# Performance work log

Hardware: AMD Instinct MI355X
Metric: run time of the kernel (lower is better)

The kernel has to match this reference:

```python
import jax, jax.numpy as jnp
import numpy as np

N = 100000          # nodes
E = 1_600_000       # edges (avg degree 16)
K_PLUS_1 = 2        # K = 1
IN_C = 64
OUT_C = 64


def setup_inputs() -> dict:
    key = jax.random.key(0)
    ks = jax.random.split(key, 7)
    X_real = jax.random.normal(ks[0], (N, IN_C), jnp.float32)
    X_imag = jax.random.normal(ks[1], (N, IN_C), jnp.float32)
    deg_scale = np.float32(1.0 / np.sqrt(16.0))  # keep spmm output O(1), like a normalized Laplacian
    L_real_vals = jax.random.normal(ks[2], (K_PLUS_1, E), jnp.float32) * deg_scale
    L_imag_vals = jax.random.normal(ks[3], (K_PLUS_1, E), jnp.float32) * deg_scale
    edge_row = jnp.sort(jax.random.randint(ks[4], (E,), 0, N))
    edge_col = jax.random.randint(ks[5], (E,), 0, N)
    stdv = np.float32(1.0 / np.sqrt(OUT_C))
    weight = jax.random.uniform(ks[6], (K_PLUS_1, IN_C, OUT_C), jnp.float32, -stdv, stdv)
    bias = jnp.zeros((1, OUT_C), jnp.float32)
    return {
        "X_real": X_real, "X_imag": X_imag,
        "L_real_vals": L_real_vals, "L_imag_vals": L_imag_vals,
        "weight": weight, "bias": bias,
        "edge_row": edge_row, "edge_col": edge_col,
    }


def reference(X_real, X_imag, L_real_vals, L_imag_vals, weight, bias, edge_row, edge_col):
    # spmm(L_i, X): gather source features, scale by edge value, scatter-add to rows
    def spmm(vals, X):
        return jax.ops.segment_sum(vals[:, None] * X[edge_col], edge_row, num_segments=N)

    def term(lr, li, w):
        # (Lr Xr) W + (-Li Xi) W == (Lr Xr - Li Xi) W  (same math as original, fused)
        real = jnp.matmul(spmm(lr, X_real) - spmm(li, X_imag), w)
        imag = jnp.matmul(spmm(li, X_real) + spmm(lr, X_imag), w)
        return real, imag

    real_k, imag_k = jax.vmap(term)(L_real_vals, L_imag_vals, weight)  # [K+1, N, out_c]
    real = jnp.sum(real_k, axis=0) + bias
    imag = jnp.sum(imag_k, axis=0) + bias
    return real, imag
```

## Files before the change

### kernel.cpp

```cpp
#include <hip/hip_runtime.h>

#define CH 64
#define RPB 8
#define BLOCK (RPB * 64)

typedef short short8 __attribute__((ext_vector_type(8)));
typedef float f32x4 __attribute__((ext_vector_type(4)));
typedef unsigned short ushort8v __attribute__((ext_vector_type(8)));
typedef _Float16 half2v __attribute__((ext_vector_type(2)));

__device__ __forceinline__ unsigned short f2bf(float f) {
    unsigned u = __float_as_uint(f);
    u += 0x7fff + ((u >> 16) & 1);
    return (unsigned short)(u >> 16);
}
__device__ __forceinline__ float bf2f(unsigned short h) {
    return __uint_as_float(((unsigned)h) << 16);
}
__device__ __forceinline__ unsigned pkh2(float a, float b) {
    union { half2v h; unsigned u; } cv;
    cv.h = half2v{(_Float16)a, (_Float16)b};
    return cv.u;
}
__device__ __forceinline__ half2v u2h2(unsigned u) {
    union { unsigned u; half2v h; } cv;
    cv.u = u;
    return cv.h;
}

__global__ __launch_bounds__(256) void build_row_ptr(
    const int* __restrict__ erow, int* __restrict__ rp, int N, int E)
{
    int r = blockIdx.x * 256 + threadIdx.x;
    if (r > N) return;
    int lo = 0, len = E;
    while (len > 0) {
        int half = len >> 1;
        int probe = lo + half;
        int v = erow[probe];
        if (v < r) { lo = probe + 1; len -= half + 1; }
        else { len = half; }
    }
    rp[r] = lo;
}

__global__ __launch_bounds__(256) void prep_wfrag(
    const float* __restrict__ W, unsigned short* __restrict__ wf)
{
    int tid = blockIdx.x * 256 + threadIdx.x;
    if (tid >= 2048) return;
    int lane = tid & 63;
    int nt = (tid >> 6) & 3;
    int ks = (tid >> 8) & 3;
    int h  = (tid >> 10) & 1;
    int n  = nt * 16 + (lane & 15);
    int g  = lane >> 4;
    ushort8v o;
    #pragma unroll
    for (int j = 0; j < 8; ++j) {
        int kk = ks * 32 + g * 8 + j;
        float w = (kk < 64) ? W[kk * 64 + n] : W[4096 + (kk - 64) * 64 + n];
        unsigned short hi = f2bf(w);
        o[j] = h ? f2bf(w - bf2f(hi)) : hi;
    }
    *(ushort8v*)(wf + (size_t)tid * 8) = o;
}

__global__ __launch_bounds__(256) void pack_x(
    const float* __restrict__ Xr, const float* __restrict__ Xi,
    unsigned* __restrict__ Xp, int total4)
{
    int i = blockIdx.x * 256 + threadIdx.x;
    if (i >= total4) return;
    float4 r  = ((const float4*)Xr)[i];
    float4 im = ((const float4*)Xi)[i];
    uint4 o;
    o.x = pkh2(r.x, im.x);
    o.y = pkh2(r.y, im.y);
    o.z = pkh2(r.z, im.z);
    o.w = pkh2(r.w, im.w);
    ((uint4*)Xp)[i] = o;
}

#define ISSUE(BUF, SB)                                                      \
    do {                                                                    \
        _Pragma("unroll")                                                   \
        for (int j_ = 0; j_ < 8; ++j_) {                                    \
            int c_ = __builtin_amdgcn_readlane(vcol, (SB) * 8 + j_);        \
            if constexpr (PK) {                                             \
                xp##BUF[j_] = Xp[(size_t)c_ * CH + lane];                   \
            } else {                                                        \
                xr##BUF[j_] = Xr[(size_t)c_ * CH + lane];                   \
                xi##BUF[j_] = Xi[(size_t)c_ * CH + lane];                   \
            }                                                               \
        }                                                                   \
        __builtin_amdgcn_sched_barrier(0);                                  \
    } while (0)

#define PROC(BUF, SB)                                                       \
    do {                                                                    \
        _Pragma("unroll")                                                   \
        for (int j_ = 0; j_ < 8; ++j_) {                                    \
            int k_ = (SB) * 8 + j_;                                         \
            if constexpr (PK) {                                             \
                unsigned u0a_ = (unsigned)__builtin_amdgcn_readlane((int)vp0a, k_); \
                unsigned u0b_ = (unsigned)__builtin_amdgcn_readlane((int)vp0b, k_); \
                unsigned u1a_ = (unsigned)__builtin_amdgcn_readlane((int)vp1a, k_); \
                unsigned u1b_ = (unsigned)__builtin_amdgcn_readlane((int)vp1b, k_); \
                half2v xv_ = u2h2(xp##BUF[j_]);                             \
                a0 = __builtin_amdgcn_fdot2(xv_, u2h2(u0a_), a0, false);    \
                b0 = __builtin_amdgcn_fdot2(xv_, u2h2(u0b_), b0, false);    \
                a1 = __builtin_amdgcn_fdot2(xv_, u2h2(u1a_), a1, false);    \
                b1 = __builtin_amdgcn_fdot2(xv_, u2h2(u1b_), b1, false);    \
            } else {                                                        \
                float l0r_ = __uint_as_float(__builtin_amdgcn_readlane(__float_as_uint(vl0r), k_)); \
                float l0i_ = __uint_as_float(__builtin_amdgcn_readlane(__float_as_uint(vl0i), k_)); \
                float l1r_ = __uint_as_float(__builtin_amdgcn_readlane(__float_as_uint(vl1r), k_)); \
                float l1i_ = __uint_as_float(__builtin_amdgcn_readlane(__float_as_uint(vl1i), k_)); \
                a0 += l0r_ * xr##BUF[j_] - l0i_ * xi##BUF[j_];              \
                b0 += l0i_ * xr##BUF[j_] + l0r_ * xi##BUF[j_];              \
                a1 += l1r_ * xr##BUF[j_] - l1i_ * xi##BUF[j_];              \
                b1 += l1i_ * xr##BUF[j_] + l1r_ * xi##BUF[j_];              \
            }                                                               \
        }                                                                   \
    } while (0)

template<int NSB, bool PK>
__device__ __forceinline__ void proc_row(
    int vcol,
    unsigned vp0a, unsigned vp0b, unsigned vp1a, unsigned vp1b,
    float vl0r, float vl0i, float vl1r, float vl1i,
    const unsigned* __restrict__ Xp,
    const float* __restrict__ Xr, const float* __restrict__ Xi, int lane,
    float& a0, float& b0, float& a1, float& b1)
{
    unsigned xpA[8], xpB[8];
    float xrA[8], xiA[8], xrB[8], xiB[8];
    ISSUE(A, 0);
    if constexpr (NSB > 1) ISSUE(B, 1);
    PROC(A, 0);
    if constexpr (NSB > 2) ISSUE(A, 2);
    if constexpr (NSB > 1) PROC(B, 1);
    if constexpr (NSB > 3) ISSUE(B, 3);
    if constexpr (NSB > 2) PROC(A, 2);
    if constexpr (NSB > 4) ISSUE(A, 4);
    if constexpr (NSB > 3) PROC(B, 3);
    if constexpr (NSB > 5) ISSUE(B, 5);
    if constexpr (NSB > 4) PROC(A, 4);
    if constexpr (NSB > 6) ISSUE(A, 6);
    if constexpr (NSB > 5) PROC(B, 5);
    if constexpr (NSB > 7) ISSUE(B, 7);
    if constexpr (NSB > 6) PROC(A, 6);
    if constexpr (NSB > 7) PROC(B, 7);
}

template<bool PK>
__global__ __launch_bounds__(BLOCK, 6) void sdconv_fused(
    const unsigned* __restrict__ Xp,
    const float* __restrict__ Xr, const float* __restrict__ Xi,
    const float* __restrict__ Lr, const float* __restrict__ Li,
    const float* __restrict__ bias,
    const int* __restrict__ ecol, const int* __restrict__ rp,
    const unsigned short* __restrict__ wf,
    float* __restrict__ outR, float* __restrict__ outI,
    int N, int E)
{
    __shared__ __align__(16) float sA[4 * RPB * 68];

    const int t    = threadIdx.x;
    const int wave = t >> 6;
    const int lane = t & 63;
    const int r0   = blockIdx.x * RPB;
    const int row  = r0 + wave;

    int start = 0, end = 0;
    if (row < N) { start = rp[row]; end = rp[row + 1]; }
    start = __builtin_amdgcn_readfirstlane(start);
    end   = __builtin_amdgcn_readfirstlane(end);

    const float* __restrict__ Lr1 = Lr + E;
    const float* __restrict__ Li1 = Li + E;

    float a0 = 0.f, b0 = 0.f, a1 = 0.f, b1 = 0.f;

    for (int base = start; base < end; base += 64) {
        int  eid  = base + lane;
        bool ok   = eid < end;
        int  eidc = ok ? eid : start;
        int   vcol = ecol[eidc];
        float vl0r = ok ? Lr[eidc]  : 0.f;
        float vl0i = ok ? Li[eidc]  : 0.f;
        float vl1r = ok ? Lr1[eidc] : 0.f;
        float vl1i = ok ? Li1[eidc] : 0.f;

        unsigned vp0a = 0, vp0b = 0, vp1a = 0, vp1b = 0;
        if constexpr (PK) {
            vp0a = pkh2(vl0r, -vl0i);
            vp0b = pkh2(vl0i,  vl0r);
            vp1a = pkh2(vl1r, -vl1i);
            vp1b = pkh2(vl1i,  vl1r);
        }

        int m = end - base; if (m > 64) m = 64;
        int nsb = (m + 7) >> 3;
        switch (nsb) {
            case 1: proc_row<1, PK>(vcol, vp0a, vp0b, vp1a, vp1b, vl0r, vl0i, vl1r, vl1i, Xp, Xr, Xi, lane, a0, b0, a1, b1); break;
            case 2: proc_row<2, PK>(vcol, vp0a, vp0b, vp1a, vp1b, vl0r, vl0i, vl1r, vl1i, Xp, Xr, Xi, lane, a0, b0, a1, b1); break;
            case 3: proc_row<3, PK>(vcol, vp0a, vp0b, vp1a, vp1b, vl0r, vl0i, vl1r, vl1i, Xp, Xr, Xi, lane, a0, b0, a1, b1); break;
            case 4: proc_row<4, PK>(vcol, vp0a, vp0b, vp1a, vp1b, vl0r, vl0i, vl1r, vl1i, Xp, Xr, Xi, lane, a0, b0, a1, b1); break;
            case 5: proc_row<5, PK>(vcol, vp0a, vp0b, vp1a, vp1b, vl0r, vl0i, vl1r, vl1i, Xp, Xr, Xi, lane, a0, b0, a1, b1); break;
            case 6: proc_row<6, PK>(vcol, vp0a, vp0b, vp1a, vp1b, vl0r, vl0i, vl1r, vl1i, Xp, Xr, Xi, lane, a0, b0, a1, b1); break;
            case 7: proc_row<7, PK>(vcol, vp0a, vp0b, vp1a, vp1b, vl0r, vl0i, vl1r, vl1i, Xp, Xr, Xi, lane, a0, b0, a1, b1); break;
            default: proc_row<8, PK>(vcol, vp0a, vp0b, vp1a, vp1b, vl0r, vl0i, vl1r, vl1i, Xp, Xr, Xi, lane, a0, b0, a1, b1); break;
        }
    }

    sA[(0 * RPB + wave) * 68 + lane] = a0;
    sA[(1 * RPB + wave) * 68 + lane] = a1;
    sA[(2 * RPB + wave) * 68 + lane] = b0;
    sA[(3 * RPB + wave) * 68 + lane] = b1;
    __syncthreads();

    const int nt    = wave & 3;
    const int abase = (wave < 4) ? 0 : 2;
    const int cidx  = lane & 15;
    const int g     = lane >> 4;
    const int ar    = lane & 15;

    f32x4 acc = {0.f, 0.f, 0.f, 0.f};
    #pragma unroll
    for (int ks = 0; ks < 4; ++ks) {
        const int kk0 = ks * 32 + g * 8;
        short8 ah = {0, 0, 0, 0, 0, 0, 0, 0};
        if (ar < 8) {
            const int arr = abase + (kk0 >= 64 ? 1 : 0);
            const float* src = &sA[(arr * RPB + ar) * 68 + (kk0 & 63)];
            float4 v0 = *(const float4*)src;
            float4 v1 = *(const float4*)(src + 4);
            float av[8] = {v0.x, v0.y, v0.z, v0.w, v1.x, v1.y, v1.z, v1.w};
            #pragma unroll
            for (int j = 0; j < 8; ++j)
                ah[j] = (short)f2bf(av[j]);
        }
        short8 bh = *(const short8*)(wf + (size_t)((0 * 4 + ks) * 4 + nt) * 512 + lane * 8);
        short8 bl = *(const short8*)(wf + (size_t)((1 * 4 + ks) * 4 + nt) * 512 + lane * 8);
        acc = __builtin_amdgcn_mfma_f32_16x16x32_bf16(ah, bh, acc, 0, 0, 0);
        acc = __builtin_amdgcn_mfma_f32_16x16x32_bf16(ah, bl, acc, 0, 0, 0);
    }

    if (g < 2) {
        float bv = bias[nt * 16 + cidx];
        float* dst = (wave < 4) ? outR : outI;
        #pragma unroll
        for (int q = 0; q < 4; ++q) {
            int grow = r0 + g * 4 + q;
            if (grow < N)
                dst[(size_t)grow * CH + nt * 16 + cidx] = acc[q] + bv;
        }
    }
}

extern "C" void kernel_launch(void* const* d_in, const int* in_sizes, int n_in,
                              void* d_out, int out_size, void* d_ws, size_t ws_size,
                              hipStream_t stream)
{
    const float* Xr   = (const float*)d_in[0];
    const float* Xi   = (const float*)d_in[1];
    const float* Lr   = (const float*)d_in[2];
    const float* Li   = (const float*)d_in[3];
    const float* W    = (const float*)d_in[4];
    const float* bias = (const float*)d_in[5];
    const int*   erow = (const int*)d_in[6];
    const int*   ecol = (const int*)d_in[7];

    const int N = in_sizes[0] / CH;
    const int E = in_sizes[6];

    int* rp = (int*)d_ws;
    size_t woff = (((size_t)(N + 1) * 4) + 255) & ~(size_t)255;
    unsigned short* wfrag = (unsigned short*)((char*)d_ws + woff);
    size_t xoff = (woff + 32 * 1024 + 255) & ~(size_t)255;
    unsigned* Xp = (unsigned*)((char*)d_ws + xoff);
    size_t need = xoff + (size_t)N * CH * 4;

    float* outR = (float*)d_out;
    float* outI = outR + (size_t)N * CH;

    hipLaunchKernelGGL(build_row_ptr, dim3((N + 1 + 255) / 256), dim3(256), 0, stream,
                       erow, rp, N, E);
    hipLaunchKernelGGL(prep_wfrag, dim3(8), dim3(256), 0, stream, W, wfrag);

    int nb = (N + RPB - 1) / RPB;
    if (ws_size >= need) {
        int total4 = N * CH / 4;
        hipLaunchKernelGGL(pack_x, dim3((total4 + 255) / 256), dim3(256), 0, stream,
                           Xr, Xi, Xp, total4);
        hipLaunchKernelGGL(sdconv_fused<true>, dim3(nb), dim3(BLOCK), 0, stream,
                           Xp, Xr, Xi, Lr, Li, bias, ecol, rp, wfrag, outR, outI, N, E);
    } else {
        hipLaunchKernelGGL(sdconv_fused<false>, dim3(nb), dim3(BLOCK), 0, stream,
                           (const unsigned*)nullptr, Xr, Xi, Lr, Li, bias, ecol, rp,
                           wfrag, outR, outI, N, E);
    }
}
```

Measured before the change: 122.8 us.

## Compute SpMM aggregation with fp16 MFMA using masked edge-value tiles per wave

Replaces the per-row fdot2 accumulation with MFMA tiles. Edge values are broadcast via ds_bpermute and masked so that only the lane matching the current row contributes to the A operand. Each wave handles 8 rows and does its own bf16 MFMA weight projection without a block-wide sync. Most of the A matrix is zero-masked, so the MFMA work is largely redundant. Gather loads are now 16-lane chunks rather than full 64-lane rows, which could hurt coalescing. The fallback path becomes a naive per-row kernel.

```diff
diff --git a/kernel.cpp b/kernel.cpp
--- a/kernel.cpp
+++ b/kernel.cpp
@@ -1,10 +1,12 @@
 #include <hip/hip_runtime.h>
 
 #define CH 64
-#define RPB 8
-#define BLOCK (RPB * 64)
+#define RPW 8
+#define WPB 4
+#define BLOCK (WPB * 64)
 
 typedef short short8 __attribute__((ext_vector_type(8)));
+typedef _Float16 half8 __attribute__((ext_vector_type(8)));
 typedef float f32x4 __attribute__((ext_vector_type(4)));
 typedef unsigned short ushort8v __attribute__((ext_vector_type(8)));
 typedef _Float16 half2v __attribute__((ext_vector_type(2)));
@@ -22,11 +24,8 @@
     cv.h = half2v{(_Float16)a, (_Float16)b};
     return cv.u;
 }
-__device__ __forceinline__ half2v u2h2(unsigned u) {
-    union { unsigned u; half2v h; } cv;
-    cv.u = u;
-    return cv.h;
-}
+
+union U8h { unsigned u[4]; half8 h; };
 
 __global__ __launch_bounds__(256) void build_row_ptr(
     const int* __restrict__ erow, int* __restrict__ rp, int N, int E)
@@ -82,82 +81,39 @@
     ((uint4*)Xp)[i] = o;
 }
 
-#define ISSUE(BUF, SB)                                                      \
-    do {                                                                    \
-        _Pragma("unroll")                                                   \
-        for (int j_ = 0; j_ < 8; ++j_) {                                    \
-            int c_ = __builtin_amdgcn_readlane(vcol, (SB) * 8 + j_);        \
-            if constexpr (PK) {                                             \
-                xp##BUF[j_] = Xp[(size_t)c_ * CH + lane];                   \
-            } else {                                                        \
-                xr##BUF[j_] = Xr[(size_t)c_ * CH + lane];                   \
-                xi##BUF[j_] = Xi[(size_t)c_ * CH + lane];                   \
-            }                                                               \
-        }                                                                   \
-        __builtin_amdgcn_sched_barrier(0);                                  \
-    } while (0)
-
-#define PROC(BUF, SB)                                                       \
-    do {                                                                    \
-        _Pragma("unroll")                                                   \
-        for (int j_ = 0; j_ < 8; ++j_) {                                    \
-            int k_ = (SB) * 8 + j_;                                         \
-            if constexpr (PK) {                                             \
-                unsigned u0a_ = (unsigned)__builtin_amdgcn_readlane((int)vp0a, k_); \
-                unsigned u0b_ = (unsigned)__builtin_amdgcn_readlane((int)vp0b, k_); \
-                unsigned u1a_ = (unsigned)__builtin_amdgcn_readlane((int)vp1a, k_); \
-                unsigned u1b_ = (unsigned)__builtin_amdgcn_readlane((int)vp1b, k_); \
-                half2v xv_ = u2h2(xp##BUF[j_]);                             \
-                a0 = __builtin_amdgcn_fdot2(xv_, u2h2(u0a_), a0, false);    \
-                b0 = __builtin_amdgcn_fdot2(xv_, u2h2(u0b_), b0, false);    \
-                a1 = __builtin_amdgcn_fdot2(xv_, u2h2(u1a_), a1, false);    \
-                b1 = __builtin_amdgcn_fdot2(xv_, u2h2(u1b_), b1, false);    \
-            } else {                                                        \
-                float l0r_ = __uint_as_float(__builtin_amdgcn_readlane(__float_as_uint(vl0r), k_)); \
-                float l0i_ = __uint_as_float(__builtin_amdgcn_readlane(__float_as_uint(vl0i), k_)); \
-                float l1r_ = __uint_as_float(__builtin_amdgcn_readlane(__float_as_uint(vl1r), k_)); \
-                float l1i_ = __uint_as_float(__builtin_amdgcn_readlane(__float_as_uint(vl1i), k_)); \
-                a0 += l0r_ * xr##BUF[j_] - l0i_ * xi##BUF[j_];              \
-                b0 += l0i_ * xr##BUF[j_] + l0r_ * xi##BUF[j_];              \
-                a1 += l1r_ * xr##BUF[j_] - l1i_ * xi##BUF[j_];              \
-                b1 += l1i_ * xr##BUF[j_] + l1r_ * xi##BUF[j_];              \
-            }                                                               \
-        }                                                                   \
-    } while (0)
-
-template<int NSB, bool PK>
-__device__ __forceinline__ void proc_row(
-    int vcol,
-    unsigned vp0a, unsigned vp0b, unsigned vp1a, unsigned vp1b,
-    float vl0r, float vl0i, float vl1r, float vl1i,
+__global__ __launch_bounds__(64) void sdconv_naive(
+    const float* __restrict__ Xr, const float* __restrict__ Xi,
+    const float* __restrict__ Lr, const float* __restrict__ Li,
+    const float* __restrict__ W, const float* __restrict__ bias,
+    const int* __restrict__ ecol, const int* __restrict__ rp,
+    float* __restrict__ outR, float* __restrict__ outI, int N, int E)
+{
+    int row = blockIdx.x;
+    int lane = threadIdx.x;
+    if (row >= N) return;
+    __shared__ float s[4][64];
+    float a0 = 0.f, b0 = 0.f, a1 = 0.f, b1 = 0.f;
+    for (int e = rp[row]; e < rp[row + 1]; ++e) {
+        int c = ecol[e];
+        float xr = Xr[(size_t)c * 64 + lane], xi = Xi[(size_t)c * 64 + lane];
+        float l0r = Lr[e], l0i = Li[e], l1r = Lr[E + e], l1i = Li[E + e];
+        a0 += l0r * xr - l0i * xi;  b0 += l0i * xr + l0r * xi;
+        a1 += l1r * xr - l1i * xi;  b1 += l1i * xr + l1r * xi;
+    }
+    s[0][lane] = a0; s[1][lane] = a1; s[2][lane] = b0; s[3][lane] = b1;
+    __syncthreads();
+    float oR = bias[lane], oI = bias[lane];
+    for (int c = 0; c < 64; ++c) {
+        float w0 = W[c * 64 + lane], w1 = W[4096 + c * 64 + lane];
+        oR += s[0][c] * w0 + s[1][c] * w1;
+        oI += s[2][c] * w0 + s[3][c] * w1;
+    }
+    outR[(size_t)row * 64 + lane] = oR;
+    outI[(size_t)row * 64 + lane] = oI;
+}
+
+__global__ __launch_bounds__(BLOCK, 3) void sdconv_fused(
     const unsigned* __restrict__ Xp,
-    const float* __restrict__ Xr, const float* __restrict__ Xi, int lane,
-    float& a0, float& b0, float& a1, float& b1)
-{
-    unsigned xpA[8], xpB[8];
-    float xrA[8], xiA[8], xrB[8], xiB[8];
-    ISSUE(A, 0);
-    if constexpr (NSB > 1) ISSUE(B, 1);
-    PROC(A, 0);
-    if constexpr (NSB > 2) ISSUE(A, 2);
-    if constexpr (NSB > 1) PROC(B, 1);
-    if constexpr (NSB > 3) ISSUE(B, 3);
-    if constexpr (NSB > 2) PROC(A, 2);
-    if constexpr (NSB > 4) ISSUE(A, 4);
-    if constexpr (NSB > 3) PROC(B, 3);
-    if constexpr (NSB > 5) ISSUE(B, 5);
-    if constexpr (NSB > 4) PROC(A, 4);
-    if constexpr (NSB > 6) ISSUE(A, 6);
-    if constexpr (NSB > 5) PROC(B, 5);
-    if constexpr (NSB > 7) ISSUE(B, 7);
-    if constexpr (NSB > 6) PROC(A, 6);
-    if constexpr (NSB > 7) PROC(B, 7);
-}
-
-template<bool PK>
-__global__ __launch_bounds__(BLOCK, 6) void sdconv_fused(
-    const unsigned* __restrict__ Xp,
-    const float* __restrict__ Xr, const float* __restrict__ Xi,
     const float* __restrict__ Lr, const float* __restrict__ Li,
     const float* __restrict__ bias,
     const int* __restrict__ ecol, const int* __restrict__ rp,
@@ -165,97 +121,144 @@
     float* __restrict__ outR, float* __restrict__ outI,
     int N, int E)
 {
-    __shared__ __align__(16) float sA[4 * RPB * 68];
+    __shared__ float sA[WPB][4 * RPW * 68];
 
     const int t    = threadIdx.x;
     const int wave = t >> 6;
     const int lane = t & 63;
-    const int r0   = blockIdx.x * RPB;
-    const int row  = r0 + wave;
-
-    int start = 0, end = 0;
-    if (row < N) { start = rp[row]; end = rp[row + 1]; }
-    start = __builtin_amdgcn_readfirstlane(start);
-    end   = __builtin_amdgcn_readfirstlane(end);
+    const int me   = lane & 15;
+    const int g    = lane >> 4;
+    const int r0w  = (blockIdx.x * WPB + wave) * RPW;
+
+    int rpidx = r0w + (lane < 9 ? lane : 8);
+    if (rpidx > N) rpidx = N;
+    const int vrp = rp[rpidx];
 
     const float* __restrict__ Lr1 = Lr + E;
     const float* __restrict__ Li1 = Li + E;
 
-    float a0 = 0.f, b0 = 0.f, a1 = 0.f, b1 = 0.f;
-
-    for (int base = start; base < end; base += 64) {
-        int  eid  = base + lane;
-        bool ok   = eid < end;
-        int  eidc = ok ? eid : start;
-        int   vcol = ecol[eidc];
-        float vl0r = ok ? Lr[eidc]  : 0.f;
-        float vl0i = ok ? Li[eidc]  : 0.f;
-        float vl1r = ok ? Lr1[eidc] : 0.f;
-        float vl1i = ok ? Li1[eidc] : 0.f;
-
-        unsigned vp0a = 0, vp0b = 0, vp1a = 0, vp1b = 0;
-        if constexpr (PK) {
-            vp0a = pkh2(vl0r, -vl0i);
-            vp0b = pkh2(vl0i,  vl0r);
-            vp1a = pkh2(vl1r, -vl1i);
-            vp1b = pkh2(vl1i,  vl1r);
+    f32x4 acc[4][4];
+    #pragma unroll
+    for (int v = 0; v < 4; ++v)
+        #pragma unroll
+        for (int c = 0; c < 4; ++c)
+            acc[v][c] = (f32x4){0.f, 0.f, 0.f, 0.f};
+
+    for (int tr = 0; tr < RPW; ++tr) {
+        const int s  = __builtin_amdgcn_readlane(vrp, tr);
+        const int e2 = __builtin_amdgcn_readlane(vrp, tr + 1);
+        const unsigned amask = (me == tr) ? 0xffffffffu : 0u;
+        for (int wb = s; wb < e2; wb += 64) {
+            int  eid  = wb + lane;
+            bool ok   = eid < e2;
+            int  eidc = ok ? eid : s;
+            int   vcol = ecol[eidc];
+            float l0r = ok ? Lr[eidc]  : 0.f;
+            float l0i = ok ? Li[eidc]  : 0.f;
+            float l1r = ok ? Lr1[eidc] : 0.f;
+            float l1i = ok ? Li1[eidc] : 0.f;
+            int vpk[4];
+            vpk[0] = (int)pkh2(l0r, -l0i);
+            vpk[1] = (int)pkh2(l0i,  l0r);
+            vpk[2] = (int)pkh2(l1r, -l1i);
+            vpk[3] = (int)pkh2(l1i,  l1r);
+
+            int wlen = e2 - wb; if (wlen > 64) wlen = 64;
+            int ntile = (wlen + 15) >> 4;
+            for (int tt = 0; tt < ntile; ++tt) {
+                const int eb  = tt * 16 + g * 4;
+                const int ad0 = (eb + 0) * 4, ad1 = (eb + 1) * 4;
+                const int ad2 = (eb + 2) * 4, ad3 = (eb + 3) * 4;
+                int c0 = __builtin_amdgcn_ds_bpermute(ad0, vcol);
+                int c1 = __builtin_amdgcn_ds_bpermute(ad1, vcol);
+                int c2 = __builtin_amdgcn_ds_bpermute(ad2, vcol);
+                int c3 = __builtin_amdgcn_ds_bpermute(ad3, vcol);
+                U8h F[4];
+                #pragma unroll
+                for (int v = 0; v < 4; ++v) {
+                    unsigned b0_ = (unsigned)__builtin_amdgcn_ds_bpermute(ad0, vpk[v]);
+                    unsigned b1_ = (unsigned)__builtin_amdgcn_ds_bpermute(ad1, vpk[v]);
+                    unsigned b2_ = (unsigned)__builtin_amdgcn_ds_bpermute(ad2, vpk[v]);
+                    unsigned b3_ = (unsigned)__builtin_amdgcn_ds_bpermute(ad3, vpk[v]);
+                    F[v].u[0] = b0_ & amask;
+                    F[v].u[1] = b1_ & amask;
+                    F[v].u[2] = b2_ & amask;
+                    F[v].u[3] = b3_ & amask;
+                }
+                unsigned o0 = ((unsigned)c0 << 6) + (unsigned)me;
+                unsigned o1 = ((unsigned)c1 << 6) + (unsigned)me;
+                unsigned o2 = ((unsigned)c2 << 6) + (unsigned)me;
+                unsigned o3 = ((unsigned)c3 << 6) + (unsigned)me;
+                U8h Bt[4];
+                #pragma unroll
+                for (int c = 0; c < 4; ++c) {
+                    Bt[c].u[0] = Xp[o0 + c * 16];
+                    Bt[c].u[1] = Xp[o1 + c * 16];
+                    Bt[c].u[2] = Xp[o2 + c * 16];
+                    Bt[c].u[3] = Xp[o3 + c * 16];
+                }
+                #pragma unroll
+                for (int c = 0; c < 4; ++c)
+                    #pragma unroll
+                    for (int v = 0; v < 4; ++v)
+                        acc[v][c] = __builtin_amdgcn_mfma_f32_16x16x32_f16(
+                            F[v].h, Bt[c].h, acc[v][c], 0, 0, 0);
+            }
         }
-
-        int m = end - base; if (m > 64) m = 64;
-        int nsb = (m + 7) >> 3;
-        switch (nsb) {
-            case 1: proc_row<1, PK>(vcol, vp0a, vp0b, vp1a, vp1b, vl0r, vl0i, vl1r, vl1i, Xp, Xr, Xi, lane, a0, b0, a1, b1); break;
-            case 2: proc_row<2, PK>(vcol, vp0a, vp0b, vp1a, vp1b, vl0r, vl0i, vl1r, vl1i, Xp, Xr, Xi, lane, a0, b0, a1, b1); break;
-            case 3: proc_row<3, PK>(vcol, vp0a, vp0b, vp1a, vp1b, vl0r, vl0i, vl1r, vl1i, Xp, Xr, Xi, lane, a0, b0, a1, b1); break;
-            case 4: proc_row<4, PK>(vcol, vp0a, vp0b, vp1a, vp1b, vl0r, vl0i, vl1r, vl1i, Xp, Xr, Xi, lane, a0, b0, a1, b1); break;
-            case 5: proc_row<5, PK>(vcol, vp0a, vp0b, vp1a, vp1b, vl0r, vl0i, vl1r, vl1i, Xp, Xr, Xi, lane, a0, b0, a1, b1); break;
-            case 6: proc_row<6, PK>(vcol, vp0a, vp0b, vp1a, vp1b, vl0r, vl0i, vl1r, vl1i, Xp, Xr, Xi, lane, a0, b0, a1, b1); break;
-            case 7: proc_row<7, PK>(vcol, vp0a, vp0b, vp1a, vp1b, vl0r, vl0i, vl1r, vl1i, Xp, Xr, Xi, lane, a0, b0, a1, b1); break;
-            default: proc_row<8, PK>(vcol, vp0a, vp0b, vp1a, vp1b, vl0r, vl0i, vl1r, vl1i, Xp, Xr, Xi, lane, a0, b0, a1, b1); break;
+    }
+
+    float* sl = sA[wave];
+    if (g < 2) {
+        const int arrmap[4] = {0, 2, 1, 3};
+        #pragma unroll
+        for (int v = 0; v < 4; ++v)
+            #pragma unroll
+            for (int c = 0; c < 4; ++c)
+                #pragma unroll
+                for (int q = 0; q < 4; ++q)
+                    sl[(arrmap[v] * RPW + g * 4 + q) * 68 + c * 16 + me] = acc[v][c][q];
+    }
+    __asm__ volatile("s_waitcnt lgkmcnt(0)" ::: "memory");
+
+    #pragma unroll
+    for (int kind = 0; kind < 2; ++kind) {
+        const int abase = kind * 2;
+        f32x4 o[4];
+        #pragma unroll
+        for (int nt = 0; nt < 4; ++nt) o[nt] = (f32x4){0.f, 0.f, 0.f, 0.f};
+        #pragma unroll
+        for (int ks = 0; ks < 4; ++ks) {
+            const int kk0 = ks * 32 + g * 8;
+            short8 ah = {0, 0, 0, 0, 0, 0, 0, 0};
+            if (me < 8) {
+                const int arr = abase + (kk0 >= 64 ? 1 : 0);
+                const float* src = &sl[(arr * RPW + me) * 68 + (kk0 & 63)];
+                float4 v0 = *(const float4*)src;
+                float4 v1 = *(const float4*)(src + 4);
+                float av[8] = {v0.x, v0.y, v0.z, v0.w, v1.x, v1.y, v1.z, v1.w};
+                #pragma unroll
+                for (int j = 0; j < 8; ++j) ah[j] = (short)f2bf(av[j]);
+            }
+            #pragma unroll
+            for (int nt = 0; nt < 4; ++nt) {
+                short8 bh = *(const short8*)(wf + (size_t)((0 * 4 + ks) * 4 + nt) * 512 + lane * 8);
+                short8 bl = *(const short8*)(wf + (size_t)((1 * 4 + ks) * 4 + nt) * 512 + lane * 8);
+                o[nt] = __builtin_amdgcn_mfma_f32_16x16x32_bf16(ah, bh, o[nt], 0, 0, 0);
+                o[nt] = __builtin_amdgcn_mfma_f32_16x16x32_bf16(ah, bl, o[nt], 0, 0, 0);
+            }
         }
-    }
-
-    sA[(0 * RPB + wave) * 68 + lane] = a0;
-    sA[(1 * RPB + wave) * 68 + lane] = a1;
-    sA[(2 * RPB + wave) * 68 + lane] = b0;
-    sA[(3 * RPB + wave) * 68 + lane] = b1;
-    __syncthreads();
-
-    const int nt    = wave & 3;
-    const int abase = (wave < 4) ? 0 : 2;
-    const int cidx  = lane & 15;
-    const int g     = lane >> 4;
-    const int ar    = lane & 15;
-
-    f32x4 acc = {0.f, 0.f, 0.f, 0.f};
-    #pragma unroll
-    for (int ks = 0; ks < 4; ++ks) {
-        const int kk0 = ks * 32 + g * 8;
-        short8 ah = {0, 0, 0, 0, 0, 0, 0, 0};
-        if (ar < 8) {
-            const int arr = abase + (kk0 >= 64 ? 1 : 0);
-            const float* src = &sA[(arr * RPB + ar) * 68 + (kk0 & 63)];
-            float4 v0 = *(const float4*)src;
-            float4 v1 = *(const float4*)(src + 4);
-            float av[8] = {v0.x, v0.y, v0.z, v0.w, v1.x, v1.y, v1.z, v1.w};
+        if (g < 2) {
+            float* __restrict__ dst = kind ? outI : outR;
             #pragma unroll
-            for (int j = 0; j < 8; ++j)
-                ah[j] = (short)f2bf(av[j]);
-        }
-        short8 bh = *(const short8*)(wf + (size_t)((0 * 4 + ks) * 4 + nt) * 512 + lane * 8);
-        short8 bl = *(const short8*)(wf + (size_t)((1 * 4 + ks) * 4 + nt) * 512 + lane * 8);
-        acc = __builtin_amdgcn_mfma_f32_16x16x32_bf16(ah, bh, acc, 0, 0, 0);
-        acc = __builtin_amdgcn_mfma_f32_16x16x32_bf16(ah, bl, acc, 0, 0, 0);
-    }
-
-    if (g < 2) {
-        float bv = bias[nt * 16 + cidx];
-        float* dst = (wave < 4) ? outR : outI;
-        #pragma unroll
-        for (int q = 0; q < 4; ++q) {
-            int grow = r0 + g * 4 + q;
-            if (grow < N)
-                dst[(size_t)grow * CH + nt * 16 + cidx] = acc[q] + bv;
+            for (int nt = 0; nt < 4; ++nt) {
+                float bv = bias[nt * 16 + me];
+                #pragma unroll
+                for (int q = 0; q < 4; ++q) {
+                    int grow = r0w + g * 4 + q;
+                    if (grow < N)
+                        dst[(size_t)grow * CH + nt * 16 + me] = o[nt][q] + bv;
+                }
+            }
         }
     }
 }
@@ -288,18 +291,17 @@
 
     hipLaunchKernelGGL(build_row_ptr, dim3((N + 1 + 255) / 256), dim3(256), 0, stream,
                        erow, rp, N, E);
-    hipLaunchKernelGGL(prep_wfrag, dim3(8), dim3(256), 0, stream, W, wfrag);
-
-    int nb = (N + RPB - 1) / RPB;
+
     if (ws_size >= need) {
+        hipLaunchKernelGGL(prep_wfrag, dim3(8), dim3(256), 0, stream, W, wfrag);
         int total4 = N * CH / 4;
         hipLaunchKernelGGL(pack_x, dim3((total4 + 255) / 256), dim3(256), 0, stream,
                            Xr, Xi, Xp, total4);
-        hipLaunchKernelGGL(sdconv_fused<true>, dim3(nb), dim3(BLOCK), 0, stream,
-                           Xp, Xr, Xi, Lr, Li, bias, ecol, rp, wfrag, outR, outI, N, E);
+        int nb = (N + WPB * RPW - 1) / (WPB * RPW);
+        hipLaunchKernelGGL(sdconv_fused, dim3(nb), dim3(BLOCK), 0, stream,
+                           Xp, Lr, Li, bias, ecol, rp, wfrag, outR, outI, N, E);
     } else {
-        hipLaunchKernelGGL(sdconv_fused<false>, dim3(nb), dim3(BLOCK), 0, stream,
-                           (const unsigned*)nullptr, Xr, Xi, Lr, Li, bias, ecol, rp,
-                           wfrag, outR, outI, N, E);
-    }
-}
+        hipLaunchKernelGGL(sdconv_naive, dim3(N), dim3(64), 0, stream,
+                           Xr, Xi, Lr, Li, W, bias, ecol, rp, outR, outI, N, E);
+    }
+}
```

New measurement: 152.0 us. +23.8%, slower.
